# Kernel tuning notes

Hardware: AMD Instinct MI355X
Metric: run time of the kernel (lower is better)

The kernel has to match this reference:

```python
import jax, jax.numpy as jnp
import numpy as np

B, T, N, DIN, U, K, C = 32, 256, 128, 16, 64, 2, 4
M = K + 1  # num diffusion matrices per support (I, P, 2P^2-I, ...)


def setup_inputs() -> dict:
    key = jax.random.key(0)
    ks = jax.random.split(key, 10)
    w = lambda k, shape: jax.random.normal(k, shape, jnp.float32) * 0.05
    inp = {}
    inp["input_seq"] = jax.random.normal(ks[0], (B, T, N, DIN), jnp.float32)
    inp["seq_lengths"] = jax.random.randint(ks[1], (B,), 1, T + 1)
    # scaled dense support (graph laplacian surrogate) for numerical stability
    inp["support"] = jax.random.normal(ks[2], (N, N), jnp.float32) / N
    inp["W0_gate"] = w(ks[3], ((DIN + U) * M, 2 * U))
    inp["b0_gate"] = jnp.ones((2 * U,), jnp.float32)  # bias_start=1.0
    inp["W0_cand"] = w(ks[4], ((DIN + U) * M, U))
    inp["b0_cand"] = jnp.zeros((U,), jnp.float32)
    inp["W1_gate"] = w(ks[5], (2 * U * M, 2 * U))
    inp["b1_gate"] = jnp.ones((2 * U,), jnp.float32)
    inp["W1_cand"] = w(ks[6], (2 * U * M, U))
    inp["b1_cand"] = jnp.zeros((U,), jnp.float32)
    inp["W_fc"] = w(ks[7], (U, C))
    inp["b_fc"] = jnp.zeros((C,), jnp.float32)
    return inp


def _gconv(x, support, W, b):
    # x: (B, N, Cin). Chebyshev-style diffusion: [x, Px, 2P(Px)-x, ...]
    x0 = x
    x1 = jnp.einsum('mn,bnc->bmc', support, x0)
    xs = [x0, x1]
    for _ in range(2, K + 1):
        x2 = 2.0 * jnp.einsum('mn,bnc->bmc', support, x1) - x0
        xs.append(x2)
        x0, x1 = x1, x2
    # stack on last axis -> (B, N, Cin, M) -> (B, N, Cin*M), matching the
    # torch reshape order (input feature major, matrix minor)
    xc = jnp.stack(xs, axis=-1).reshape(x.shape[0], x.shape[1], -1)
    return xc @ W + b


def _cell(x, h, support, Wg, bg, Wc, bc):
    # x: (B,N,Din), h: (B,N,U)
    val = jax.nn.sigmoid(_gconv(jnp.concatenate([x, h], axis=-1), support, Wg, bg))
    r, u = jnp.split(val, 2, axis=-1)
    c = jnp.tanh(_gconv(jnp.concatenate([x, r * h], axis=-1), support, Wc, bc))
    return u * h + (1.0 - u) * c


def _run_layer(x_seq, support, Wg, bg, Wc, bc):
    # x_seq: (T, B, N, D)
    def step(h, x):
        h2 = _cell(x, h, support, Wg, bg, Wc, bc)
        return h2, h2
    h0 = jnp.zeros((x_seq.shape[1], N, U), x_seq.dtype)
    _, out = jax.lax.scan(step, h0, x_seq)
    return out  # (T, B, N, U)


def reference(input_seq, seq_lengths, support, W0_gate, b0_gate, W0_cand, b0_cand,
              W1_gate, b1_gate, W1_cand, b1_cand, W_fc, b_fc):
    x = jnp.transpose(input_seq, (1, 0, 2, 3))  # (T,B,N,DIN)
    h1 = _run_layer(x, support, W0_gate, b0_gate, W0_cand, b0_cand)
    h2 = _run_layer(h1, support, W1_gate, b1_gate, W1_cand, b1_cand)
    out_seq = jnp.transpose(h2, (1, 0, 2, 3))  # (B,T,N,U)
    idx = seq_lengths - 1  # last relevant timestep per sequence
    last = out_seq[jnp.arange(out_seq.shape[0]), idx]  # (B,N,U)
    # dropout is identity in eval mode
    logits = jax.nn.relu(last) @ W_fc + b_fc  # (B,N,C)
    return jnp.max(logits, axis=1)  # max-pool over nodes -> (B,C)
```

## Files before the change

### kernel.cpp

```cpp
#include <hip/hip_runtime.h>

#define B_   32
#define T_   256
#define N_   128
#define DIN_ 16
#define U_   64

#define PD 456
#define PT 136
#define LDS_BYTES ((N_*PD + N_*PT)*2)

#define WT0G_OFF 0
#define WT0C_OFF (128*256)
#define WT1G_OFF (WT0C_OFF + 64*256)
#define WT1C_OFF (WT1G_OFF + 128*384)
#define WT_TOTAL (WT1C_OFF + 64*384)
#define S2_OFF   WT_TOTAL
#define FIFO2_OFF (S2_OFF + 128*128)
#define FIFO2_SLOT(bb,tt) (FIFO2_OFF + ((bb)*4 + ((tt)&3))*24576)
#define FLG_BYTE ((FIFO2_OFF + 32*4*24576)*2)

typedef __attribute__((ext_vector_type(8))) short bfrag;
typedef __attribute__((ext_vector_type(4))) float ffrag;
typedef __attribute__((ext_vector_type(4))) unsigned short us4;
typedef __attribute__((ext_vector_type(2))) unsigned short us2;
typedef unsigned long long ull;

#define SYNC() asm volatile("s_waitcnt lgkmcnt(0)\n\ts_barrier" ::: "memory")
#define MFMA16(a,b,c) __builtin_amdgcn_mfma_f32_16x16x32_bf16(a,b,c,0,0,0)

__device__ __forceinline__ unsigned short f2b(float x) {
  union { float f; unsigned u; } v; v.f = x;
  return (unsigned short)((v.u + 0x7fffu + ((v.u >> 16) & 1u)) >> 16);
}
__device__ __forceinline__ float sigm(float x) {
  float e = __expf(-x);
  return __builtin_amdgcn_rcpf(1.f + e);
}
__device__ __forceinline__ float tanh_(float x) {
  float e = __expf(2.f * x);
  return 1.f - 2.f * __builtin_amdgcn_rcpf(1.f + e);
}

__device__ __forceinline__ float wval0(const float* w, int ncol, int co, int k) {
  if (k < 16)  return w[(k*3+0)*ncol+co] - w[(k*3+2)*ncol+co];
  if (k < 48)  { int j=k-16, c=j>>1;
                 return (j&1) ? 2.f*w[(c*3+2)*ncol+co] : w[(c*3+1)*ncol+co]; }
  if (k < 64)  return 0.f;
  if (k < 128) { int c=16+(k-64); return w[(c*3+0)*ncol+co] - w[(c*3+2)*ncol+co]; }
  { int j=k-128, c=16+(j>>1);
    return (j&1) ? 2.f*w[(c*3+2)*ncol+co] : w[(c*3+1)*ncol+co]; }
}
__device__ __forceinline__ float wval1(const float* w, int ncol, int co, int k) {
  if (k < 64)  return w[(k*3+0)*ncol+co] - w[(k*3+2)*ncol+co];
  if (k < 192) { int j=k-64, c=j>>1;
                 return (j&1) ? 2.f*w[(c*3+2)*ncol+co] : w[(c*3+1)*ncol+co]; }
  if (k < 256) { int c=64+(k-192); return w[(c*3+0)*ncol+co] - w[(c*3+2)*ncol+co]; }
  { int j=k-256, c=64+(j>>1);
    return (j&1) ? 2.f*w[(c*3+2)*ncol+co] : w[(c*3+1)*ncol+co]; }
}
__device__ __forceinline__ float wval0c(const float* w, int ncol, int co, int k) {
  if (k < 64)  return wval0(w, ncol, co, k);
  if (k < 192) return wval0(w, ncol, co, k + 64);
  return wval0(w, ncol, co, k - 128);
}
__device__ __forceinline__ float wval1c(const float* w, int ncol, int co, int k) {
  if (k < 192) return wval1(w, ncol, co, k);
  if (k < 320) return wval1(w, ncol, co, k + 64);
  return wval1(w, ncol, co, k - 128);
}

__global__ void setup_wt(const float* __restrict__ w0g, const float* __restrict__ w0c,
                         const float* __restrict__ w1g, const float* __restrict__ w1c,
                         unsigned short* __restrict__ wt) {
  int i = blockIdx.x * blockDim.x + threadIdx.x;
  if (i >= WT_TOTAL) return;
  float v;
  if (i < WT0C_OFF)      { int co = i >> 8, k = i & 255;                 v = wval0 (w0g, 128, co, k); }
  else if (i < WT1G_OFF) { int j = i - WT0C_OFF; v = wval0c(w0c, 64, j >> 8, j & 255); }
  else if (i < WT1C_OFF) { int j = i - WT1G_OFF; v = wval1 (w1g, 128, j / 384, j % 384); }
  else                   { int j = i - WT1C_OFF; v = wval1c(w1c, 64, j / 384, j % 384); }
  wt[i] = f2b(v);
}

__global__ void setup_s2(const float* __restrict__ sup, unsigned short* __restrict__ s2) {
  int idx = blockIdx.x * blockDim.x + threadIdx.x;
  int i = idx >> 7, j = idx & 127;
  float acc = 0.f;
#pragma unroll 4
  for (int k = 0; k < 128; ++k) acc += sup[i*128 + k] * sup[k*128 + j];
  s2[idx] = f2b(acc);
}

__global__ void zero_flags(unsigned short* __restrict__ wt) {
  int* flg = (int*)((char*)wt + FLG_BYTE);
  if (threadIdx.x < 64) flg[threadIdx.x] = 0;
}

template<int KT>
__device__ __forceinline__ void gateR(ffrag (&acc)[4][2],
    const bfrag (&bwr)[KT], const bfrag (&bwu)[KT],
    const unsigned short* __restrict__ arowB, const int lq) {
#pragma unroll
  for (int ks = 0; ks < KT; ++ks) {
    bfrag a[4];
#pragma unroll
    for (int i = 0; i < 4; ++i)
      a[i] = *(const bfrag*)&arowB[16*i*PD + 32*ks + 8*lq];
#pragma unroll
    for (int i = 0; i < 4; ++i) {
      acc[i][0] = MFMA16(a[i], bwr[ks], acc[i][0]);
      acc[i][1] = MFMA16(a[i], bwu[ks], acc[i][1]);
    }
  }
}
template<int KT>
__device__ __forceinline__ void candR(ffrag (&acc)[4], bfrag (&bw)[4],
    const unsigned short* __restrict__ arowB, const int (&kofs)[KT],
    const unsigned short* __restrict__ bpc, const int lq) {
#pragma unroll
  for (int ks = 0; ks < KT; ++ks) {
    const int k = ks & 3;
    bfrag a[4];
#pragma unroll
    for (int i = 0; i < 4; ++i)
      a[i] = *(const bfrag*)&arowB[16*i*PD + kofs[ks] + 8*lq];
    bfrag bc = bw[k];
    if (ks + 4 < KT) bw[k] = *(const bfrag*)&bpc[32*(ks+4) + 8*lq];
#pragma unroll
    for (int i = 0; i < 4; ++i) acc[i] = MFMA16(a[i], bc, acc[i]);
  }
}

__global__ __launch_bounds__(512, 2) void dcgru(
    const float* __restrict__ xseq, const int* __restrict__ slen,
    const float* __restrict__ sup,
    const float* __restrict__ b0g, const float* __restrict__ b0c,
    const float* __restrict__ b1g, const float* __restrict__ b1c,
    const float* __restrict__ wfc, const float* __restrict__ bfc,
    unsigned short* __restrict__ wt, float* __restrict__ out) {
  extern __shared__ unsigned short lds[];
  unsigned short* diffb = lds;
  unsigned short* difT  = lds + N_*PD;
  const int b    = (blockIdx.x & 7) | ((blockIdx.x >> 4) << 3);
  const int eta  = (blockIdx.x >> 3) & 1;
  const int tid  = threadIdx.x;
  const int w    = tid >> 6;
  const int j    = w & 3;
  const int g    = w >> 2;
  const int ln   = tid & 15;
  const int lq   = (tid >> 4) & 3;
  const int L    = slen[b];
  int* flg  = (int*)((char*)wt + FLG_BYTE);
  int* prod = flg + b;
  int* cons = flg + 32 + b;
  const unsigned short* __restrict__ arowB = diffb + (64*g + ln)*PD;
  const ffrag fz = {0.f, 0.f, 0.f, 0.f};
  const int fnode = tid & 127;
  const int fkb   = tid >> 7;

  bfrag Sf[4], S2f[4];
#pragma unroll
  for (int ks = 0; ks < 4; ++ks) {
    const float* pS = sup + (16*w + ln)*N_ + 32*ks + 8*lq;
    union { bfrag v; unsigned short u[8]; } tmp;
#pragma unroll
    for (int jj = 0; jj < 8; ++jj) tmp.u[jj] = f2b(pS[jj]);
    Sf[ks] = tmp.v;
    S2f[ks] = *(const bfrag*)&wt[S2_OFF + (16*w + ln)*N_ + 32*ks + 8*lq];
  }

  auto diffuse = [&](int nt, int colc) {
    bfrag bf[4];
#pragma unroll
    for (int ks = 0; ks < 4; ++ks)
      bf[ks] = *(const bfrag*)&difT[(16*nt + ln)*PT + 32*ks + 8*lq];
    ffrag a1 = fz, a2 = fz;
#pragma unroll
    for (int ks = 0; ks < 4; ++ks) {
      a1 = MFMA16(Sf[ks],  bf[ks], a1);
      a2 = MFMA16(S2f[ks], bf[ks], a2);
    }
    const int n0 = 16*w + 4*lq;
    const int col = colc + 2*ln;
#pragma unroll
    for (int r = 0; r < 4; ++r) {
      us2 pq = {f2b(a1[r]), f2b(a2[r])};
      *(us2*)&diffb[(n0 + r)*PD + col] = pq;
    }
  };
  auto dumpCell = [&](ffrag (&v)[4], int colBase, int rowBase) {
    const int chh = 16*j + ln;
#pragma unroll
    for (int i = 0; i < 4; ++i) {
      const int n0 = 64*g + 16*i + 4*lq;
      unsigned short sv[4];
#pragma unroll
      for (int r = 0; r < 4; ++r) sv[r] = f2b(v[i][r]);
#pragma unroll
      for (int r = 0; r < 4; ++r) diffb[(n0 + r)*PD + colBase + chh] = sv[r];
      us4 q = {sv[0], sv[1], sv[2], sv[3]};
      *(us4*)&difT[(rowBase + chh)*PT + n0] = q;
    }
  };
  auto prebC = [&](bfrag (&bw)[4], const unsigned short* bpc) {
#pragma unroll
    for (int k = 0; k < 4; ++k) bw[k] = *(const bfrag*)&bpc[32*k + 8*lq];
  };
  auto waitge = [&](int* p, int seq) {
    if ((tid & 63) == 0) {
      int it = 0;
      while (__hip_atomic_load(p, __ATOMIC_RELAXED, __HIP_MEMORY_SCOPE_AGENT) < seq) {
        __builtin_amdgcn_s_sleep(1);
        if (++it > (1 << 24)) break;
      }
    }
  };

  bfrag bw4[4];

  if (eta == 0) {
    bfrag bwr[8], bwu[8];
    {
      const unsigned short* bpr = wt + WT0G_OFF + (16*j      + ln)*256;
      const unsigned short* bpu = wt + WT0G_OFF + (16*(4+j)  + ln)*256;
#pragma unroll
      for (int ks = 0; ks < 8; ++ks) {
        bwr[ks] = *(const bfrag*)&bpr[32*ks + 8*lq];
        bwu[ks] = *(const bfrag*)&bpu[32*ks + 8*lq];
      }
    }
    const unsigned short* bpc = wt + WT0C_OFF + (16*j + ln)*256;
    const float bgr = b0g[16*j + ln], bgu = b0g[64 + 16*j + ln];
    const float bcv = b0c[16*j + ln];
    const int kofs0[8] = {0, 32, 128, 160, 192, 224, 256, 288};
    ffrag h0m[4] = {fz, fz, fz, fz};

    auto stageX = [&](float4 v) {
      const int node = tid >> 2, c = 4*(tid & 3);
      unsigned short s0 = f2b(v.x), s1 = f2b(v.y), s2 = f2b(v.z), s3 = f2b(v.w);
      us4 q = {s0, s1, s2, s3};
      *(us4*)&diffb[node*PD + c] = q;
      difT[(c+0)*PT + node] = s0; difT[(c+1)*PT + node] = s1;
      difT[(c+2)*PT + node] = s2; difT[(c+3)*PT + node] = s3;
    };

    for (int i = tid; i < N_*208; i += 512) {
      int row = i / 208, c = i - row*208;
      diffb[row*PD + 48 + c] = 0;
    }
    float4 xv = *(const float4*)&xseq[(size_t)(b*T_)*N_*DIN_ + 4*tid];
    stageX(xv);
    { int tn = 1 < L ? 1 : L - 1;
      xv = *(const float4*)&xseq[(size_t)(b*T_ + tn)*N_*DIN_ + 4*tid]; }
    SYNC();
    diffuse(0, 16);
    SYNC();

#pragma clang loop unroll(disable)
    for (int t = 0; t < L; ++t) {
      ffrag u0s[4], rh[4];
      {
        ffrag ga[4][2] = {{fz, fz}, {fz, fz}, {fz, fz}, {fz, fz}};
        gateR<8>(ga, bwr, bwu, arowB, lq);
#pragma unroll
        for (int i = 0; i < 4; ++i)
#pragma unroll
          for (int r = 0; r < 4; ++r) {
            float rr = sigm(ga[i][0][r] + bgr);
            rh[i][r]  = rr * h0m[i][r];
            u0s[i][r] = sigm(ga[i][1][r] + bgu);
          }
      }
      dumpCell(rh, 256, 16);
      prebC(bw4, bpc);
      SYNC();
      diffuse(1, 128); diffuse(2, 160); diffuse(3, 192); diffuse(4, 224);
      SYNC();
      {
        ffrag ca[4] = {fz, fz, fz, fz};
        candR<8>(ca, bw4, arowB, kofs0, bpc, lq);
#pragma unroll
        for (int i = 0; i < 4; ++i)
#pragma unroll
          for (int r = 0; r < 4; ++r) {
            float cc = tanh_(ca[i][r] + bcv);
            float uu = u0s[i][r];
            h0m[i][r] = uu*h0m[i][r] + (1.f - uu)*cc;
          }
      }
      dumpCell(h0m, 64, 16);
      if (t >= 4) waitge(cons, 8*(t - 3));
      SYNC();
      diffuse(1, 128); diffuse(2, 160); diffuse(3, 192); diffuse(4, 224);
      stageX(xv);
      { int tn = t + 2 < L ? t + 2 : L - 1;
        xv = *(const float4*)&xseq[(size_t)(b*T_ + tn)*N_*DIN_ + 4*tid]; }
      SYNC();
      diffuse(0, 16);
      {
        unsigned short* slot2 = wt + FIFO2_SLOT(b, t);
#pragma unroll
        for (int r = 0; r < 12; ++r) {
          const int k = fkb + 4*r;
          ull v = *(const ull*)&diffb[fnode*PD + 64 + 4*k];
          *(ull*)&slot2[k*128*4 + fnode*4] = v;
        }
      }
      asm volatile("s_waitcnt vmcnt(0)" ::: "memory");
      if ((tid & 63) == 0)
        __hip_atomic_fetch_add(prod, 1, __ATOMIC_RELEASE, __HIP_MEMORY_SCOPE_AGENT);
      SYNC();
    }
    return;
  }

  {
    bfrag bwr[12], bwu[12];
    {
      const unsigned short* bpr = wt + WT1G_OFF + (16*j     + ln)*384;
      const unsigned short* bpu = wt + WT1G_OFF + (16*(4+j) + ln)*384;
#pragma unroll
      for (int ks = 0; ks < 12; ++ks) {
        bwr[ks] = *(const bfrag*)&bpr[32*ks + 8*lq];
        bwu[ks] = *(const bfrag*)&bpu[32*ks + 8*lq];
      }
    }
    const unsigned short* bpc = wt + WT1C_OFF + (16*j + ln)*384;
    const float bgr = b1g[16*j + ln], bgu = b1g[64 + 16*j + ln];
    const float bcv = b1c[16*j + ln];
    const int kofs1[12] = {0, 32, 64, 96, 128, 160, 256, 288, 320, 352, 384, 416};
    ffrag h1m[4] = {fz, fz, fz, fz};

    auto recvSlot = [&](int t) {
      const unsigned short* slot2 = wt + FIFO2_SLOT(b, t);
#pragma unroll
      for (int r = 0; r < 12; ++r) {
        const int k = fkb + 4*r;
        ull v = __hip_atomic_load((const ull*)&slot2[k*128*4 + fnode*4],
                                  __ATOMIC_RELAXED, __HIP_MEMORY_SCOPE_AGENT);
        *(ull*)&diffb[fnode*PD + 4*k] = v;
      }
      asm volatile("s_waitcnt vmcnt(0)" ::: "memory");
      if ((tid & 63) == 0)
        __hip_atomic_fetch_add(cons, 1, __ATOMIC_RELEASE, __HIP_MEMORY_SCOPE_AGENT);
    };

    for (int i = tid; i < N_*192; i += 512) {
      int row = i / 192, c = i - row*192;
      diffb[row*PD + 192 + c] = 0;
    }
    waitge(prod, 8);
    recvSlot(0);
    SYNC();

#pragma clang loop unroll(disable)
    for (int t = 0; t < L; ++t) {
      ffrag u1s[4], rh[4];
      {
        ffrag ga[4][2] = {{fz, fz}, {fz, fz}, {fz, fz}, {fz, fz}};
        gateR<12>(ga, bwr, bwu, arowB, lq);
#pragma unroll
        for (int i = 0; i < 4; ++i)
#pragma unroll
          for (int r = 0; r < 4; ++r) {
            float rr = sigm(ga[i][0][r] + bgr);
            rh[i][r]  = rr * h1m[i][r];
            u1s[i][r] = sigm(ga[i][1][r] + bgu);
          }
      }
      dumpCell(rh, 384, 64);
      prebC(bw4, bpc);
      SYNC();
      diffuse(4, 256); diffuse(5, 288); diffuse(6, 320); diffuse(7, 352);
      SYNC();
      {
        ffrag ca[4] = {fz, fz, fz, fz};
        candR<12>(ca, bw4, arowB, kofs1, bpc, lq);
#pragma unroll
        for (int i = 0; i < 4; ++i)
#pragma unroll
          for (int r = 0; r < 4; ++r) {
            float cc = tanh_(ca[i][r] + bcv);
            float uu = u1s[i][r];
            h1m[i][r] = uu*h1m[i][r] + (1.f - uu)*cc;
          }
      }
      dumpCell(h1m, 192, 64);
      SYNC();
      diffuse(4, 256); diffuse(5, 288); diffuse(6, 320); diffuse(7, 352);
      if (t + 1 < L) {
        waitge(prod, 8*(t + 2));
        recvSlot(t + 1);
      }
      SYNC();
    }

    {
      float* hb = (float*)lds;
#pragma unroll
      for (int i = 0; i < 4; ++i)
#pragma unroll
        for (int r = 0; r < 4; ++r) {
          float v = h1m[i][r];
          hb[(64*g + 16*i + 4*lq + r)*U_ + 16*j + ln] = v > 0.f ? v : 0.f;
        }
    }
    __syncthreads();
    float* hb = (float*)lds;
    float* lb = hb + N_*U_;
    if (tid < N_) {
      float lg[4];
#pragma unroll
      for (int jj = 0; jj < 4; ++jj) lg[jj] = bfc[jj];
      for (int ch = 0; ch < U_; ++ch) {
        float v = hb[tid*U_ + ch];
#pragma unroll
        for (int jj = 0; jj < 4; ++jj) lg[jj] += v * wfc[ch*4 + jj];
      }
#pragma unroll
      for (int jj = 0; jj < 4; ++jj) lb[tid*4 + jj] = lg[jj];
    }
    __syncthreads();
    if (tid < 4) {
      float m = lb[tid];
      for (int n = 1; n < N_; ++n) m = fmaxf(m, lb[n*4 + tid]);
      out[b*4 + tid] = m;
    }
  }
}

extern "C" void kernel_launch(void* const* d_in, const int* in_sizes, int n_in,
                              void* d_out, int out_size, void* d_ws, size_t ws_size,
                              hipStream_t stream) {
  const float* xseq = (const float*)d_in[0];
  const int*   slen = (const int*)  d_in[1];
  const float* sup  = (const float*)d_in[2];
  const float* w0g  = (const float*)d_in[3];
  const float* b0g  = (const float*)d_in[4];
  const float* w0c  = (const float*)d_in[5];
  const float* b0c  = (const float*)d_in[6];
  const float* w1g  = (const float*)d_in[7];
  const float* b1g  = (const float*)d_in[8];
  const float* w1c  = (const float*)d_in[9];
  const float* b1c  = (const float*)d_in[10];
  const float* wfc  = (const float*)d_in[11];
  const float* bfc  = (const float*)d_in[12];
  float* out = (float*)d_out;
  unsigned short* wt = (unsigned short*)d_ws;

  (void)hipFuncSetAttribute((const void*)dcgru,
                            hipFuncAttributeMaxDynamicSharedMemorySize, LDS_BYTES);
  zero_flags<<<dim3(1), dim3(64), 0, stream>>>(wt);
  setup_wt<<<dim3((WT_TOTAL + 255)/256), dim3(256), 0, stream>>>(w0g, w0c, w1g, w1c, wt);
  setup_s2<<<dim3(64), dim3(256), 0, stream>>>(sup, wt + S2_OFF);
  dcgru<<<dim3(64), dim3(512), LDS_BYTES, stream>>>(
      xseq, slen, sup, b0g, b0c, b1g, b1c, wfc, bfc, wt, out);
}
```

Before: 3.044 ms.

## Fuse both GRU layers into one workgroup per batch, dropping cross-block FIFO

Previously each batch element used two workgroups: one computed layer 0 and streamed its hidden state through a global-memory FIFO with atomic flags to a second workgroup computing layer 1. Now a single workgroup per batch runs both layers back to back within each timestep, sharing one LDS buffer. Gate weights are no longer held in registers for the whole run; they are streamed from global memory with a four-deep register prefetch. This removes the global round-trip, the spin-waits and the flag kernel, but it serialises the two layers and halves the number of active workgroups, so the two layers no longer run concurrently.

```diff
diff --git a/kernel.cpp b/kernel.cpp
--- a/kernel.cpp
+++ b/kernel.cpp
@@ -6,9 +6,10 @@
 #define DIN_ 16
 #define U_   64
 
-#define PD 456
+#define PD 520
 #define PT 136
-#define LDS_BYTES ((N_*PD + N_*PT)*2)
+#define DT_ROWS 80
+#define LDS_BYTES ((N_*PD + DT_ROWS*PT)*2)
 
 #define WT0G_OFF 0
 #define WT0C_OFF (128*256)
@@ -16,9 +17,6 @@
 #define WT1C_OFF (WT1G_OFF + 128*384)
 #define WT_TOTAL (WT1C_OFF + 64*384)
 #define S2_OFF   WT_TOTAL
-#define FIFO2_OFF (S2_OFF + 128*128)
-#define FIFO2_SLOT(bb,tt) (FIFO2_OFF + ((bb)*4 + ((tt)&3))*24576)
-#define FLG_BYTE ((FIFO2_OFF + 32*4*24576)*2)
 
 typedef __attribute__((ext_vector_type(8))) short bfrag;
 typedef __attribute__((ext_vector_type(4))) float ffrag;
@@ -92,25 +90,27 @@
   s2[idx] = f2b(acc);
 }
 
-__global__ void zero_flags(unsigned short* __restrict__ wt) {
-  int* flg = (int*)((char*)wt + FLG_BYTE);
-  if (threadIdx.x < 64) flg[threadIdx.x] = 0;
-}
-
 template<int KT>
-__device__ __forceinline__ void gateR(ffrag (&acc)[4][2],
-    const bfrag (&bwr)[KT], const bfrag (&bwu)[KT],
-    const unsigned short* __restrict__ arowB, const int lq) {
+__device__ __forceinline__ void gateO(ffrag (&acc)[4][2],
+    bfrag (&br)[4], bfrag (&bu)[4],
+    const unsigned short* __restrict__ bpr, const unsigned short* __restrict__ bpu,
+    const unsigned short* __restrict__ arowB, const int (&kofs)[KT], const int lq) {
 #pragma unroll
   for (int ks = 0; ks < KT; ++ks) {
+    const int k = ks & 3;
     bfrag a[4];
 #pragma unroll
     for (int i = 0; i < 4; ++i)
-      a[i] = *(const bfrag*)&arowB[16*i*PD + 32*ks + 8*lq];
+      a[i] = *(const bfrag*)&arowB[16*i*PD + kofs[ks] + 8*lq];
+    bfrag rc = br[k], uc = bu[k];
+    if (ks + 4 < KT) {
+      br[k] = *(const bfrag*)&bpr[32*(ks+4) + 8*lq];
+      bu[k] = *(const bfrag*)&bpu[32*(ks+4) + 8*lq];
+    }
 #pragma unroll
     for (int i = 0; i < 4; ++i) {
-      acc[i][0] = MFMA16(a[i], bwr[ks], acc[i][0]);
-      acc[i][1] = MFMA16(a[i], bwu[ks], acc[i][1]);
+      acc[i][0] = MFMA16(a[i], rc, acc[i][0]);
+      acc[i][1] = MFMA16(a[i], uc, acc[i][1]);
     }
   }
 }
@@ -142,8 +142,7 @@
   extern __shared__ unsigned short lds[];
   unsigned short* diffb = lds;
   unsigned short* difT  = lds + N_*PD;
-  const int b    = (blockIdx.x & 7) | ((blockIdx.x >> 4) << 3);
-  const int eta  = (blockIdx.x >> 3) & 1;
+  const int b    = blockIdx.x;
   const int tid  = threadIdx.x;
   const int w    = tid >> 6;
   const int j    = w & 3;
@@ -151,13 +150,8 @@
   const int ln   = tid & 15;
   const int lq   = (tid >> 4) & 3;
   const int L    = slen[b];
-  int* flg  = (int*)((char*)wt + FLG_BYTE);
-  int* prod = flg + b;
-  int* cons = flg + 32 + b;
   const unsigned short* __restrict__ arowB = diffb + (64*g + ln)*PD;
   const ffrag fz = {0.f, 0.f, 0.f, 0.f};
-  const int fnode = tid & 127;
-  const int fkb   = tid >> 7;
 
   bfrag Sf[4], S2f[4];
 #pragma unroll
@@ -189,7 +183,7 @@
       *(us2*)&diffb[(n0 + r)*PD + col] = pq;
     }
   };
-  auto dumpCell = [&](ffrag (&v)[4], int colBase, int rowBase) {
+  auto dumpCell = [&](ffrag (&v)[4], int colBase) {
     const int chh = 16*j + ln;
 #pragma unroll
     for (int i = 0; i < 4; ++i) {
@@ -200,233 +194,160 @@
 #pragma unroll
       for (int r = 0; r < 4; ++r) diffb[(n0 + r)*PD + colBase + chh] = sv[r];
       us4 q = {sv[0], sv[1], sv[2], sv[3]};
-      *(us4*)&difT[(rowBase + chh)*PT + n0] = q;
+      *(us4*)&difT[(16 + chh)*PT + n0] = q;
     }
   };
-  auto prebC = [&](bfrag (&bw)[4], const unsigned short* bpc) {
-#pragma unroll
-    for (int k = 0; k < 4; ++k) bw[k] = *(const bfrag*)&bpc[32*k + 8*lq];
+  auto preb4 = [&](bfrag (&bw)[4], const unsigned short* bp) {
+#pragma unroll
+    for (int k = 0; k < 4; ++k) bw[k] = *(const bfrag*)&bp[32*k + 8*lq];
   };
-  auto waitge = [&](int* p, int seq) {
-    if ((tid & 63) == 0) {
-      int it = 0;
-      while (__hip_atomic_load(p, __ATOMIC_RELAXED, __HIP_MEMORY_SCOPE_AGENT) < seq) {
-        __builtin_amdgcn_s_sleep(1);
-        if (++it > (1 << 24)) break;
+  auto stageX = [&](float4 v) {
+    const int node = tid >> 2, c = 4*(tid & 3);
+    unsigned short s0 = f2b(v.x), s1 = f2b(v.y), s2 = f2b(v.z), s3 = f2b(v.w);
+    us4 q = {s0, s1, s2, s3};
+    *(us4*)&diffb[node*PD + c] = q;
+    difT[(c+0)*PT + node] = s0; difT[(c+1)*PT + node] = s1;
+    difT[(c+2)*PT + node] = s2; difT[(c+3)*PT + node] = s3;
+  };
+
+  const unsigned short* bpr0 = wt + WT0G_OFF + (16*j      + ln)*256;
+  const unsigned short* bpu0 = wt + WT0G_OFF + (16*(4+j)  + ln)*256;
+  const unsigned short* bpc0 = wt + WT0C_OFF + (16*j + ln)*256;
+  const unsigned short* bpr1 = wt + WT1G_OFF + (16*j     + ln)*384;
+  const unsigned short* bpu1 = wt + WT1G_OFF + (16*(4+j) + ln)*384;
+  const unsigned short* bpc1 = wt + WT1C_OFF + (16*j + ln)*384;
+  const float bgr0 = b0g[16*j + ln], bgu0 = b0g[64 + 16*j + ln], bcv0 = b0c[16*j + ln];
+  const float bgr1 = b1g[16*j + ln], bgu1 = b1g[64 + 16*j + ln], bcv1 = b1c[16*j + ln];
+
+  const int kofsG0[8]  = {0, 32, 64, 96, 128, 160, 192, 224};
+  const int kofs0[8]   = {0, 32, 128, 160, 192, 224, 256, 288};
+  const int kofsG1[12] = {64, 96, 128, 160, 192, 224, 320, 352, 384, 416, 448, 480};
+  const int kofsC1[12] = {64, 96, 128, 160, 192, 224, 384, 416, 448, 480, 256, 288};
+
+  ffrag h0m[4] = {fz, fz, fz, fz}, h1m[4] = {fz, fz, fz, fz};
+  bfrag brg[4], bug[4], bw4[4];
+
+  for (int i = tid; i < N_*464; i += 512) {
+    int row = i / 464, c = i - row*464;
+    diffb[row*PD + 48 + c] = 0;
+  }
+  float4 xv = *(const float4*)&xseq[(size_t)(b*T_)*N_*DIN_ + 4*tid];
+  stageX(xv);
+  { int tn = 1 < L ? 1 : L - 1;
+    xv = *(const float4*)&xseq[(size_t)(b*T_ + tn)*N_*DIN_ + 4*tid]; }
+  preb4(brg, bpr0); preb4(bug, bpu0);
+  SYNC();
+  diffuse(0, 16);
+  SYNC();
+
+#pragma clang loop unroll(disable)
+  for (int t = 0; t < L; ++t) {
+    ffrag u0s[4], rh[4];
+    {
+      ffrag ga[4][2] = {{fz, fz}, {fz, fz}, {fz, fz}, {fz, fz}};
+      gateO<8>(ga, brg, bug, bpr0, bpu0, arowB, kofsG0, lq);
+#pragma unroll
+      for (int i = 0; i < 4; ++i)
+#pragma unroll
+        for (int r = 0; r < 4; ++r) {
+          float rr = sigm(ga[i][0][r] + bgr0);
+          rh[i][r]  = rr * h0m[i][r];
+          u0s[i][r] = sigm(ga[i][1][r] + bgu0);
+        }
+    }
+    dumpCell(rh, 256);
+    preb4(bw4, bpc0);
+    SYNC();
+    diffuse(1, 128); diffuse(2, 160); diffuse(3, 192); diffuse(4, 224);
+    SYNC();
+    {
+      ffrag ca[4] = {fz, fz, fz, fz};
+      candR<8>(ca, bw4, arowB, kofs0, bpc0, lq);
+#pragma unroll
+      for (int i = 0; i < 4; ++i)
+#pragma unroll
+        for (int r = 0; r < 4; ++r) {
+          float cc = tanh_(ca[i][r] + bcv0);
+          float uu = u0s[i][r];
+          h0m[i][r] = uu*h0m[i][r] + (1.f - uu)*cc;
+        }
+    }
+    dumpCell(h0m, 64);
+    SYNC();
+    preb4(brg, bpr1); preb4(bug, bpu1);
+    diffuse(1, 128); diffuse(2, 160); diffuse(3, 192); diffuse(4, 224);
+    stageX(xv);
+    { int tn = t + 2 < L ? t + 2 : L - 1;
+      xv = *(const float4*)&xseq[(size_t)(b*T_ + tn)*N_*DIN_ + 4*tid]; }
+    SYNC();
+    diffuse(0, 16);
+    ffrag u1s[4], rh1[4];
+    {
+      ffrag ga[4][2] = {{fz, fz}, {fz, fz}, {fz, fz}, {fz, fz}};
+      gateO<12>(ga, brg, bug, bpr1, bpu1, arowB, kofsG1, lq);
+#pragma unroll
+      for (int i = 0; i < 4; ++i)
+#pragma unroll
+        for (int r = 0; r < 4; ++r) {
+          float rr = sigm(ga[i][0][r] + bgr1);
+          rh1[i][r] = rr * h1m[i][r];
+          u1s[i][r] = sigm(ga[i][1][r] + bgu1);
+        }
+    }
+    dumpCell(rh1, 256);
+    preb4(bw4, bpc1);
+    SYNC();
+    diffuse(1, 384); diffuse(2, 416); diffuse(3, 448); diffuse(4, 480);
+    SYNC();
+    {
+      ffrag ca[4] = {fz, fz, fz, fz};
+      candR<12>(ca, bw4, arowB, kofsC1, bpc1, lq);
+#pragma unroll
+      for (int i = 0; i < 4; ++i)
+#pragma unroll
+        for (int r = 0; r < 4; ++r) {
+          float cc = tanh_(ca[i][r] + bcv1);
+          float uu = u1s[i][r];
+          h1m[i][r] = uu*h1m[i][r] + (1.f - uu)*cc;
+        }
+    }
+    dumpCell(h1m, 320);
+    SYNC();
+    preb4(brg, bpr0); preb4(bug, bpu0);
+    diffuse(1, 384); diffuse(2, 416); diffuse(3, 448); diffuse(4, 480);
+    SYNC();
+  }
+
+  {
+    float* hb = (float*)lds;
+#pragma unroll
+    for (int i = 0; i < 4; ++i)
+#pragma unroll
+      for (int r = 0; r < 4; ++r) {
+        float v = h1m[i][r];
+        hb[(64*g + 16*i + 4*lq + r)*U_ + 16*j + ln] = v > 0.f ? v : 0.f;
       }
-    }
-  };
-
-  bfrag bw4[4];
-
-  if (eta == 0) {
-    bfrag bwr[8], bwu[8];
-    {
-      const unsigned short* bpr = wt + WT0G_OFF + (16*j      + ln)*256;
-      const unsigned short* bpu = wt + WT0G_OFF + (16*(4+j)  + ln)*256;
-#pragma unroll
-      for (int ks = 0; ks < 8; ++ks) {
-        bwr[ks] = *(const bfrag*)&bpr[32*ks + 8*lq];
-        bwu[ks] = *(const bfrag*)&bpu[32*ks + 8*lq];
-      }
-    }
-    const unsigned short* bpc = wt + WT0C_OFF + (16*j + ln)*256;
-    const float bgr = b0g[16*j + ln], bgu = b0g[64 + 16*j + ln];
-    const float bcv = b0c[16*j + ln];
-    const int kofs0[8] = {0, 32, 128, 160, 192, 224, 256, 288};
-    ffrag h0m[4] = {fz, fz, fz, fz};
-
-    auto stageX = [&](float4 v) {
-      const int node = tid >> 2, c = 4*(tid & 3);
-      unsigned short s0 = f2b(v.x), s1 = f2b(v.y), s2 = f2b(v.z), s3 = f2b(v.w);
-      us4 q = {s0, s1, s2, s3};
-      *(us4*)&diffb[node*PD + c] = q;
-      difT[(c+0)*PT + node] = s0; difT[(c+1)*PT + node] = s1;
-      difT[(c+2)*PT + node] = s2; difT[(c+3)*PT + node] = s3;
-    };
-
-    for (int i = tid; i < N_*208; i += 512) {
-      int row = i / 208, c = i - row*208;
-      diffb[row*PD + 48 + c] = 0;
-    }
-    float4 xv = *(const float4*)&xseq[(size_t)(b*T_)*N_*DIN_ + 4*tid];
-    stageX(xv);
-    { int tn = 1 < L ? 1 : L - 1;
-      xv = *(const float4*)&xseq[(size_t)(b*T_ + tn)*N_*DIN_ + 4*tid]; }
-    SYNC();
-    diffuse(0, 16);
-    SYNC();
-
-#pragma clang loop unroll(disable)
-    for (int t = 0; t < L; ++t) {
-      ffrag u0s[4], rh[4];
-      {
-        ffrag ga[4][2] = {{fz, fz}, {fz, fz}, {fz, fz}, {fz, fz}};
-        gateR<8>(ga, bwr, bwu, arowB, lq);
-#pragma unroll
-        for (int i = 0; i < 4; ++i)
-#pragma unroll
-          for (int r = 0; r < 4; ++r) {
-            float rr = sigm(ga[i][0][r] + bgr);
-            rh[i][r]  = rr * h0m[i][r];
-            u0s[i][r] = sigm(ga[i][1][r] + bgu);
-          }
-      }
-      dumpCell(rh, 256, 16);
-      prebC(bw4, bpc);
-      SYNC();
-      diffuse(1, 128); diffuse(2, 160); diffuse(3, 192); diffuse(4, 224);
-      SYNC();
-      {
-        ffrag ca[4] = {fz, fz, fz, fz};
-        candR<8>(ca, bw4, arowB, kofs0, bpc, lq);
-#pragma unroll
-        for (int i = 0; i < 4; ++i)
-#pragma unroll
-          for (int r = 0; r < 4; ++r) {
-            float cc = tanh_(ca[i][r] + bcv);
-            float uu = u0s[i][r];
-            h0m[i][r] = uu*h0m[i][r] + (1.f - uu)*cc;
-          }
-      }
-      dumpCell(h0m, 64, 16);
-      if (t >= 4) waitge(cons, 8*(t - 3));
-      SYNC();
-      diffuse(1, 128); diffuse(2, 160); diffuse(3, 192); diffuse(4, 224);
-      stageX(xv);
-      { int tn = t + 2 < L ? t + 2 : L - 1;
-        xv = *(const float4*)&xseq[(size_t)(b*T_ + tn)*N_*DIN_ + 4*tid]; }
-      SYNC();
-      diffuse(0, 16);
-      {
-        unsigned short* slot2 = wt + FIFO2_SLOT(b, t);
-#pragma unroll
-        for (int r = 0; r < 12; ++r) {
-          const int k = fkb + 4*r;
-          ull v = *(const ull*)&diffb[fnode*PD + 64 + 4*k];
-          *(ull*)&slot2[k*128*4 + fnode*4] = v;
-        }
-      }
-      asm volatile("s_waitcnt vmcnt(0)" ::: "memory");
-      if ((tid & 63) == 0)
-        __hip_atomic_fetch_add(prod, 1, __ATOMIC_RELEASE, __HIP_MEMORY_SCOPE_AGENT);
-      SYNC();
-    }
-    return;
-  }
-
-  {
-    bfrag bwr[12], bwu[12];
-    {
-      const unsigned short* bpr = wt + WT1G_OFF + (16*j     + ln)*384;
-      const unsigned short* bpu = wt + WT1G_OFF + (16*(4+j) + ln)*384;
-#pragma unroll
-      for (int ks = 0; ks < 12; ++ks) {
-        bwr[ks] = *(const bfrag*)&bpr[32*ks + 8*lq];
-        bwu[ks] = *(const bfrag*)&bpu[32*ks + 8*lq];
-      }
-    }
-    const unsigned short* bpc = wt + WT1C_OFF + (16*j + ln)*384;
-    const float bgr = b1g[16*j + ln], bgu = b1g[64 + 16*j + ln];
-    const float bcv = b1c[16*j + ln];
-    const int kofs1[12] = {0, 32, 64, 96, 128, 160, 256, 288, 320, 352, 384, 416};
-    ffrag h1m[4] = {fz, fz, fz, fz};
-
-    auto recvSlot = [&](int t) {
-      const unsigned short* slot2 = wt + FIFO2_SLOT(b, t);
-#pragma unroll
-      for (int r = 0; r < 12; ++r) {
-        const int k = fkb + 4*r;
-        ull v = __hip_atomic_load((const ull*)&slot2[k*128*4 + fnode*4],
-                                  __ATOMIC_RELAXED, __HIP_MEMORY_SCOPE_AGENT);
-        *(ull*)&diffb[fnode*PD + 4*k] = v;
-      }
-      asm volatile("s_waitcnt vmcnt(0)" ::: "memory");
-      if ((tid & 63) == 0)
-        __hip_atomic_fetch_add(cons, 1, __ATOMIC_RELEASE, __HIP_MEMORY_SCOPE_AGENT);
-    };
-
-    for (int i = tid; i < N_*192; i += 512) {
-      int row = i / 192, c = i - row*192;
-      diffb[row*PD + 192 + c] = 0;
-    }
-    waitge(prod, 8);
-    recvSlot(0);
-    SYNC();
-
-#pragma clang loop unroll(disable)
-    for (int t = 0; t < L; ++t) {
-      ffrag u1s[4], rh[4];
-      {
-        ffrag ga[4][2] = {{fz, fz}, {fz, fz}, {fz, fz}, {fz, fz}};
-        gateR<12>(ga, bwr, bwu, arowB, lq);
-#pragma unroll
-        for (int i = 0; i < 4; ++i)
-#pragma unroll
-          for (int r = 0; r < 4; ++r) {
-            float rr = sigm(ga[i][0][r] + bgr);
-            rh[i][r]  = rr * h1m[i][r];
-            u1s[i][r] = sigm(ga[i][1][r] + bgu);
-          }
-      }
-      dumpCell(rh, 384, 64);
-      prebC(bw4, bpc);
-      SYNC();
-      diffuse(4, 256); diffuse(5, 288); diffuse(6, 320); diffuse(7, 352);
-      SYNC();
-      {
-        ffrag ca[4] = {fz, fz, fz, fz};
-        candR<12>(ca, bw4, arowB, kofs1, bpc, lq);
-#pragma unroll
-        for (int i = 0; i < 4; ++i)
-#pragma unroll
-          for (int r = 0; r < 4; ++r) {
-            float cc = tanh_(ca[i][r] + bcv);
-            float uu = u1s[i][r];
-            h1m[i][r] = uu*h1m[i][r] + (1.f - uu)*cc;
-          }
-      }
-      dumpCell(h1m, 192, 64);
-      SYNC();
-      diffuse(4, 256); diffuse(5, 288); diffuse(6, 320); diffuse(7, 352);
-      if (t + 1 < L) {
-        waitge(prod, 8*(t + 2));
-        recvSlot(t + 1);
-      }
-      SYNC();
-    }
-
-    {
-      float* hb = (float*)lds;
-#pragma unroll
-      for (int i = 0; i < 4; ++i)
-#pragma unroll
-        for (int r = 0; r < 4; ++r) {
-          float v = h1m[i][r];
-          hb[(64*g + 16*i + 4*lq + r)*U_ + 16*j + ln] = v > 0.f ? v : 0.f;
-        }
-    }
-    __syncthreads();
-    float* hb = (float*)lds;
-    float* lb = hb + N_*U_;
-    if (tid < N_) {
-      float lg[4];
-#pragma unroll
-      for (int jj = 0; jj < 4; ++jj) lg[jj] = bfc[jj];
-      for (int ch = 0; ch < U_; ++ch) {
-        float v = hb[tid*U_ + ch];
-#pragma unroll
-        for (int jj = 0; jj < 4; ++jj) lg[jj] += v * wfc[ch*4 + jj];
-      }
-#pragma unroll
-      for (int jj = 0; jj < 4; ++jj) lb[tid*4 + jj] = lg[jj];
-    }
-    __syncthreads();
-    if (tid < 4) {
-      float m = lb[tid];
-      for (int n = 1; n < N_; ++n) m = fmaxf(m, lb[n*4 + tid]);
-      out[b*4 + tid] = m;
-    }
+  }
+  __syncthreads();
+  float* hb = (float*)lds;
+  float* lb = hb + N_*U_;
+  if (tid < N_) {
+    float lg[4];
+#pragma unroll
+    for (int jj = 0; jj < 4; ++jj) lg[jj] = bfc[jj];
+    for (int ch = 0; ch < U_; ++ch) {
+      float v = hb[tid*U_ + ch];
+#pragma unroll
+      for (int jj = 0; jj < 4; ++jj) lg[jj] += v * wfc[ch*4 + jj];
+    }
+#pragma unroll
+    for (int jj = 0; jj < 4; ++jj) lb[tid*4 + jj] = lg[jj];
+  }
+  __syncthreads();
+  if (tid < 4) {
+    float m = lb[tid];
+    for (int n = 1; n < N_; ++n) m = fmaxf(m, lb[n*4 + tid]);
+    out[b*4 + tid] = m;
   }
 }
 
@@ -451,9 +372,8 @@
 
   (void)hipFuncSetAttribute((const void*)dcgru,
                             hipFuncAttributeMaxDynamicSharedMemorySize, LDS_BYTES);
-  zero_flags<<<dim3(1), dim3(64), 0, stream>>>(wt);
   setup_wt<<<dim3((WT_TOTAL + 255)/256), dim3(256), 0, stream>>>(w0g, w0c, w1g, w1c, wt);
   setup_s2<<<dim3(64), dim3(256), 0, stream>>>(sup, wt + S2_OFF);
-  dcgru<<<dim3(64), dim3(512), LDS_BYTES, stream>>>(
+  dcgru<<<dim3(32), dim3(512), LDS_BYTES, stream>>>(
       xseq, slen, sup, b0g, b0c, b1g, b1c, wfc, bfc, wt, out);
 }
```

Result: slower. 4.492 ms (+47.6%).
